# Optimization experiments

Measured on AMD Instinct MI355X. Metric: run time of the kernel, lower is better.

Reference implementation:

```python
import jax, jax.numpy as jnp
import numpy as np

EMBED_DIM = 1024
NUM_HEADS = 16
HEAD_DIM = EMBED_DIM // NUM_HEADS
ROPE_BASE = 10000.0


def rotate_half(x):
    # interleaved variant: pairs (x0,x1) -> (-x1, x0)
    x1 = x[..., ::2]
    x2 = x[..., 1::2]
    return jnp.stack((-x2, x1), axis=-1).reshape(x.shape)


def rope_tables(T, dim, dtype):
    inv_freq = 1.0 / (ROPE_BASE ** (jnp.arange(0, dim, 2, dtype=jnp.float32) / dim))
    t = jnp.arange(T, dtype=jnp.float32)
    freqs = t[:, None] * inv_freq[None, :]          # [T, dim/2]
    emb = jnp.concatenate((freqs, freqs), axis=-1)  # [T, dim]
    return jnp.cos(emb).astype(dtype), jnp.sin(emb).astype(dtype)


def setup_inputs() -> dict:
    key = jax.random.key(0)
    kx, kq, ko = jax.random.split(key, 3)
    B, T, D = 2, 2048, EMBED_DIM
    x = jax.random.normal(kx, (B, T, D), dtype=jnp.float32)
    s = 1.0 / np.sqrt(D)
    Wqkv = jax.random.normal(kq, (D, 3 * D), dtype=jnp.float32) * s
    Wout = jax.random.normal(ko, (D, D), dtype=jnp.float32) * s
    return {"x": x, "Wqkv": Wqkv, "Wout": Wout}


def reference(x, Wqkv, Wout):
    B, T, D = x.shape
    H, hd = NUM_HEADS, HEAD_DIM
    qkv = x @ Wqkv                                   # [B,T,3D]
    q, k, v = jnp.split(qkv, 3, axis=-1)
    q = q.reshape(B, T, H, hd).transpose(0, 2, 1, 3)  # [B,H,T,hd]
    k = k.reshape(B, T, H, hd).transpose(0, 2, 1, 3)
    v = v.reshape(B, T, H, hd).transpose(0, 2, 1, 3)
    cos, sin = rope_tables(T, hd, x.dtype)           # [T,hd]
    cos = cos[None, None, :, :]
    sin = sin[None, None, :, :]
    q = q * cos + rotate_half(q) * sin
    k = k * cos + rotate_half(k) * sin
    scale = 1.0 / np.sqrt(hd).astype(np.float32)
    attn = jnp.einsum('bhtd,bhsd->bhts', q, k) * scale  # [B,H,T,T]
    attn = jax.nn.softmax(attn, axis=-1)
    out = jnp.einsum('bhts,bhsd->bhtd', attn, v)     # [B,H,T,hd]
    out = out.transpose(0, 2, 1, 3).reshape(B, T, D)
    return out @ Wout
```

## Files before the change

### kernel.cpp

```cpp
#include <hip/hip_runtime.h>
#include <hip/hip_bf16.h>
#include <stdint.h>


typedef unsigned short u16;
typedef short bf16x8 __attribute__((ext_vector_type(8)));
typedef float f32x4  __attribute__((ext_vector_type(4)));

#if defined(__has_builtin) && __has_builtin(__builtin_amdgcn_exp2f)
#define EXP2F(x) __builtin_amdgcn_exp2f(x)
#else
#define EXP2F(x) exp2f(x)
#endif

__device__ __forceinline__ u16 f2b(float f) {
  uint32_t u = __float_as_uint(f);
  u += 0x7fffu + ((u >> 16) & 1u);
  return (u16)(u >> 16);
}
__device__ __forceinline__ uint32_t pk2(float a, float b) {
  return (uint32_t)f2b(a) | ((uint32_t)f2b(b) << 16);
}
__device__ __forceinline__ uint32_t pkbf(float a, float b) {
  __hip_bfloat162 h = __float22bfloat162_rn(make_float2(a, b));
  union { __hip_bfloat162 h2; uint32_t u; } cv; cv.h2 = h;
  return cv.u;
}

__device__ __forceinline__ void gl2lds16(const void* g, void* l) {
  __builtin_amdgcn_global_load_lds(
      (const __attribute__((address_space(1))) unsigned int*)g,
      (__attribute__((address_space(3))) unsigned int*)l, 16, 0, 0);
}

__global__ void sniff_kernel(const u16* x, int* flag) {
  __shared__ int cnt;
  if (threadIdx.x == 0) cnt = 0;
  __syncthreads();
  int c = 0;
  for (int i = threadIdx.x; i < 4096; i += 256) {
    float a = fabsf(__uint_as_float(((uint32_t)x[2*i]) << 16));
    if (a > 1e-3f && a < 100.f) c++;
  }
  atomicAdd(&cnt, c);
  __syncthreads();
  if (threadIdx.x == 0) *flag = (cnt > 2048) ? 1 : 0;
}

__device__ __forceinline__ void tr_tile(const void* src, u16* dst, int Kd, int N,
                                        int n0, int k0, int isb, u16* Lt, int tid)
{
  const int r = tid >> 2, cseg = (tid & 3) << 4;
  u16 t[16];
  if (isb) {
    const u16* s = (const u16*)src + (size_t)(k0 + r) * N + n0 + cseg;
    *(uint4*)&t[0] = *(const uint4*)s;
    *(uint4*)&t[8] = *(const uint4*)(s + 8);
  } else {
    const float* s = (const float*)src + (size_t)(k0 + r) * N + n0 + cseg;
    #pragma unroll
    for (int j = 0; j < 4; j++) {
      float4 v = *(const float4*)(s + j * 4);
      t[j*4+0] = f2b(v.x); t[j*4+1] = f2b(v.y); t[j*4+2] = f2b(v.z); t[j*4+3] = f2b(v.w);
    }
  }
  #pragma unroll
  for (int j = 0; j < 16; j++) Lt[(cseg + j) * 72 + r] = t[j];
  __syncthreads();
  const int n = tid >> 2, kseg = (tid & 3) << 4;
  uint4 u0 = *(const uint4*)&Lt[n * 72 + kseg];
  uint4 u1 = *(const uint4*)&Lt[n * 72 + kseg + 8];
  u16* d = dst + (size_t)(n0 + n) * Kd + k0 + kseg;
  *(uint4*)d = u0;
  *(uint4*)(d + 8) = u1;
}

__global__ __launch_bounds__(256) void prep_kernel(
    const void* __restrict__ x, const void* __restrict__ wqkv,
    const void* __restrict__ wout, const int* __restrict__ flag,
    u16* __restrict__ Xb, u16* __restrict__ Wqkvt, u16* __restrict__ Woutt,
    float2* __restrict__ CS)
{
  __shared__ u16 Lt[64 * 72];
  const int isb = *flag;
  const int bid = blockIdx.x, tid = threadIdx.x;
  if (bid < 2048) {
    const size_t i = ((size_t)bid * 256 + tid) * 8;
    if (isb) {
      *(uint4*)&Xb[i] = *(const uint4*)((const u16*)x + i);
    } else {
      const float* s = (const float*)x + i;
      float4 a = *(const float4*)s, b = *(const float4*)(s + 4);
      uint4 p;
      p.x = pkbf(a.x, a.y); p.y = pkbf(a.z, a.w);
      p.z = pkbf(b.x, b.y); p.w = pkbf(b.z, b.w);
      *(uint4*)&Xb[i] = p;
    }
  } else if (bid < 2816) {
    const int b = bid - 2048;
    tr_tile(wqkv, Wqkvt, 1024, 3072, (b % 48) * 64, (b / 48) * 64, isb, Lt, tid);
  } else if (bid < 3072) {
    const int b = bid - 2816;
    tr_tile(wout, Woutt, 1024, 1024, (b % 16) * 64, (b / 16) * 64, isb, Lt, tid);
  } else {
    const int idx = (bid - 3072) * 256 + tid;
    const int t = idx >> 5, f = idx & 31;
    float invf = __expf(-(float)f * 0.2878231366242557f);
    float th = (float)t * invf;
    float sn, cs;
    sincosf(th, &sn, &cs);
    CS[idx] = make_float2(cs, sn);
  }
}

__global__ __launch_bounds__(256) void qkv_kernel(
    const u16* __restrict__ Xb, const u16* __restrict__ Wt,
    const float2* __restrict__ CS,
    u16* __restrict__ Q, u16* __restrict__ K, u16* __restrict__ Vt)
{
  __shared__ u16 As[128 * 64];
  __shared__ u16 Bs[128 * 64];
  const int tid = threadIdx.x;
  const int n0 = blockIdx.x * 128;
  const int m0 = blockIdx.y * 128;
  const int w = tid >> 6, l = tid & 63, lr = l & 15, lq = l >> 4;
  const int mrow0 = (w & 1) * 64;
  const int ncol0 = (w >> 1) * 64;
  const int srow = tid >> 3;
  const int gseg = (tid & 7) ^ (srow & 7);

  f32x4 acc[4][4] = {};

  for (int k0 = 0; k0 < 1024; k0 += 64) {
    __syncthreads();
    #pragma unroll
    for (int rd = 0; rd < 4; rd++) {
      const int row = srow + rd * 32;
      gl2lds16(Xb + (size_t)(m0 + row) * 1024 + k0 + gseg * 8, &As[tid * 8 + rd * 2048]);
      gl2lds16(Wt + (size_t)(n0 + row) * 1024 + k0 + gseg * 8, &Bs[tid * 8 + rd * 2048]);
    }
    __syncthreads();
    #pragma unroll
    for (int kc = 0; kc < 2; kc++) {
      bf16x8 af[4], bf[4];
      #pragma unroll
      for (int i = 0; i < 4; i++) {
        const int seg = ((kc << 2) | lq) ^ (lr & 7);
        af[i] = *(const bf16x8*)&As[(mrow0 + i * 16 + lr) * 64 + seg * 8];
        bf[i] = *(const bf16x8*)&Bs[(ncol0 + i * 16 + lr) * 64 + seg * 8];
      }
      #pragma unroll
      for (int mb = 0; mb < 4; mb++)
        #pragma unroll
        for (int nb = 0; nb < 4; nb++)
          acc[mb][nb] = __builtin_amdgcn_mfma_f32_16x16x32_bf16(af[mb], bf[nb], acc[mb][nb], 0, 0, 0);
    }
  }

  const int col0 = n0 + ncol0;
  const int sec = col0 >> 10;
  const int h = (col0 >> 6) & 15;
  if (sec == 2) {
    #pragma unroll
    for (int mb = 0; mb < 4; mb++) {
      const int row0 = m0 + mrow0 + mb * 16 + lq * 4;
      const int b = row0 >> 11, t0 = row0 & 2047;
      #pragma unroll
      for (int nb = 0; nb < 4; nb++) {
        const int d = nb * 16 + lr;
        uint2 uv;
        uv.x = pkbf(acc[mb][nb][0], acc[mb][nb][1]);
        uv.y = pkbf(acc[mb][nb][2], acc[mb][nb][3]);
        *(uint2*)&Vt[(((size_t)b * 16 + h) * 64 + d) * 2048 + t0] = uv;
      }
    }
  } else {
    u16* dst = (sec == 0) ? Q : K;
    const float qscale = 0.125f * 1.44269504f;
    #pragma unroll
    for (int mb = 0; mb < 4; mb++) {
      const int row0 = m0 + mrow0 + mb * 16 + lq * 4;
      const int b = row0 >> 11, t0 = row0 & 2047;
      #pragma unroll
      for (int nb = 0; nb < 4; nb++) {
        const int d = nb * 16 + lr;
        const int f = d & 31;
        #pragma unroll
        for (int r = 0; r < 4; r++) {
          const int t = t0 + r;
          float2 cs = CS[t * 32 + f];
          float val = acc[mb][nb][r];
          float prt = __shfl_xor(val, 1, 64);
          float res = fmaf(val, cs.x, ((d & 1) ? prt : -prt) * cs.y);
          if (sec == 0) res *= qscale;
          dst[(((size_t)b * 16 + h) * 2048 + t) * 64 + d] = f2b(res);
        }
      }
    }
  }
}

__global__ __launch_bounds__(256, 2) void attn_kernel(
    const u16* __restrict__ Q, const u16* __restrict__ K,
    const u16* __restrict__ Vt, u16* __restrict__ ATT,
    float* __restrict__ Op, float* __restrict__ Ls)
{
  __shared__ u16 Ks[2][64 * 64];
  __shared__ u16 Vs[2][64 * 64];
  __shared__ u16 Ps[4][64 * 64];
  const int tid = threadIdx.x;
  const int w = tid >> 6, l = tid & 63, lr = l & 15, lq = l >> 4;
  const int bh = blockIdx.x >> 3;
  const int qt = blockIdx.x & 7;
  const int ns = gridDim.y, sh = blockIdx.y;
  const int slen = 2048 / ns;
  const int sbeg = sh * slen;
  const size_t base = (size_t)bh * (2048 * 64);
  const int qrow0 = qt * 256 + w * 64;
  u16* Psw = &Ps[w][0];

  bf16x8 qf[4][2];
  #pragma unroll
  for (int mb = 0; mb < 4; mb++)
    #pragma unroll
    for (int kc = 0; kc < 2; kc++)
      qf[mb][kc] = *(const bf16x8*)(Q + base + (size_t)(qrow0 + mb * 16 + lr) * 64 + kc * 32 + lq * 8);

  f32x4 oa[4][4] = {};
  float lsum[4] = {0.f, 0.f, 0.f, 0.f};

  const int srow = tid >> 3;

  auto stage = [&](int buf, int s0) {
    #pragma unroll
    for (int rd = 0; rd < 2; rd++) {
      const int row = srow + rd * 32;
      const int gs = (tid & 7) ^ (row & 7);
      gl2lds16(K + base + (size_t)(s0 + row) * 64 + gs * 8, &Ks[buf][tid * 8 + rd * 2048]);
      gl2lds16(Vt + base + (size_t)row * 2048 + s0 + gs * 8, &Vs[buf][tid * 8 + rd * 2048]);
    }
  };

  stage(0, sbeg);
  const int nt = slen >> 6;

  #pragma unroll 1
  for (int t = 0; t < nt; t++) {
    const int buf = t & 1;
    __syncthreads();
    if (t + 1 < nt) stage(buf ^ 1, sbeg + (t + 1) * 64);

    bf16x8 kf[4][2], vf[4][2];
    #pragma unroll
    for (int nb = 0; nb < 4; nb++)
      #pragma unroll
      for (int kc = 0; kc < 2; kc++) {
        const int seg = ((kc << 2) | lq) ^ (lr & 7);
        kf[nb][kc] = *(const bf16x8*)&Ks[buf][(nb * 16 + lr) * 64 + seg * 8];
        vf[nb][kc] = *(const bf16x8*)&Vs[buf][(nb * 16 + lr) * 64 + seg * 8];
      }

    #pragma unroll
    for (int sb = 0; sb < 4; sb++) {
      #pragma unroll
      for (int mb = 0; mb < 4; mb++) {
        f32x4 st = {};
        st = __builtin_amdgcn_mfma_f32_16x16x32_bf16(kf[sb][0], qf[mb][0], st, 0, 0, 0);
        st = __builtin_amdgcn_mfma_f32_16x16x32_bf16(kf[sb][1], qf[mb][1], st, 0, 0, 0);
        float e0 = EXP2F(st[0]), e1 = EXP2F(st[1]), e2 = EXP2F(st[2]), e3 = EXP2F(st[3]);
        lsum[mb] += (e0 + e1) + (e2 + e3);
        uint2 pp;
        pp.x = pkbf(e0, e1);
        pp.y = pkbf(e2, e3);
        const int pseg = ((sb << 1) | (lq >> 1)) ^ (lr & 7);
        *(uint2*)&Psw[(mb * 16 + lr) * 64 + pseg * 8 + (lq & 1) * 4] = pp;
      }
    }

    #pragma unroll
    for (int mb = 0; mb < 4; mb++) {
      const int rs0 = lq ^ (lr & 7);
      const int rs1 = (4 | lq) ^ (lr & 7);
      bf16x8 pf0 = *(const bf16x8*)&Psw[(mb * 16 + lr) * 64 + rs0 * 8];
      bf16x8 pf1 = *(const bf16x8*)&Psw[(mb * 16 + lr) * 64 + rs1 * 8];
      #pragma unroll
      for (int db = 0; db < 4; db++) {
        oa[db][mb] = __builtin_amdgcn_mfma_f32_16x16x32_bf16(vf[db][0], pf0, oa[db][mb], 0, 0, 0);
        oa[db][mb] = __builtin_amdgcn_mfma_f32_16x16x32_bf16(vf[db][1], pf1, oa[db][mb], 0, 0, 0);
      }
    }
  }

  #pragma unroll
  for (int mb = 0; mb < 4; mb++) {
    float v = lsum[mb];
    v += __shfl_xor(v, 16, 64);
    v += __shfl_xor(v, 32, 64);
    lsum[mb] = v;
  }

  const int b = bh >> 4, h = bh & 15;
  if (ns == 1) {
    #pragma unroll
    for (int mb = 0; mb < 4; mb++) {
      const float inv = 1.f / lsum[mb];
      const int t = qrow0 + mb * 16 + lr;
      u16* dst = ATT + ((size_t)(b * 2048 + t)) * 1024 + h * 64;
      #pragma unroll
      for (int db = 0; db < 4; db++) {
        uint2 u;
        u.x = pkbf(oa[db][mb][0] * inv, oa[db][mb][1] * inv);
        u.y = pkbf(oa[db][mb][2] * inv, oa[db][mb][3] * inv);
        *(uint2*)&dst[db * 16 + lq * 4] = u;
      }
    }
  } else {
    float* op = Op + (size_t)sh * (65536ull * 64);
    #pragma unroll
    for (int mb = 0; mb < 4; mb++) {
      const size_t row = (size_t)bh * 2048 + qrow0 + mb * 16 + lr;
      #pragma unroll
      for (int db = 0; db < 4; db++)
        *(f32x4*)&op[row * 64 + db * 16 + lq * 4] = oa[db][mb];
      if (lq == 0) Ls[(size_t)sh * 65536 + row] = lsum[mb];
    }
  }
}

__global__ __launch_bounds__(256) void combine_kernel(
    const float* __restrict__ Op, const float* __restrict__ Ls, u16* __restrict__ ATT)
{
  const int idx = blockIdx.x * 256 + threadIdx.x;
  const int R = idx >> 3;
  const int c = (idx & 7) * 8;
  const float* p0 = Op + (size_t)R * 64 + c;
  const float* p1 = p0 + 65536ull * 64;
  f32x4 a0 = *(const f32x4*)p0, a1 = *(const f32x4*)(p0 + 4);
  f32x4 b0 = *(const f32x4*)p1, b1 = *(const f32x4*)(p1 + 4);
  const float inv = 1.f / (Ls[R] + Ls[65536 + R]);
  const int bh = R >> 11, trow = R & 2047;
  const int b = bh >> 4, h = bh & 15;
  u16* d = ATT + ((size_t)(b * 2048 + trow)) * 1024 + h * 64 + c;
  uint4 u;
  u.x = pkbf((a0[0] + b0[0]) * inv, (a0[1] + b0[1]) * inv);
  u.y = pkbf((a0[2] + b0[2]) * inv, (a0[3] + b0[3]) * inv);
  u.z = pkbf((a1[0] + b1[0]) * inv, (a1[1] + b1[1]) * inv);
  u.w = pkbf((a1[2] + b1[2]) * inv, (a1[3] + b1[3]) * inv);
  *(uint4*)d = u;
}

__global__ __launch_bounds__(256) void outproj_kernel(
    const u16* __restrict__ A, const u16* __restrict__ Wt,
    const int* __restrict__ flag, void* __restrict__ outv)
{
  __shared__ u16 As[128 * 64];
  __shared__ u16 Bs[128 * 64];
  const int isb = *flag;
  const int tid = threadIdx.x;
  const int n0 = blockIdx.x * 128;
  const int m0 = blockIdx.y * 128;
  const int w = tid >> 6, l = tid & 63, lr = l & 15, lq = l >> 4;
  const int mrow0 = (w & 1) * 64;
  const int ncol0 = (w >> 1) * 64;
  const int srow = tid >> 3;
  const int gseg = (tid & 7) ^ (srow & 7);

  f32x4 acc[4][4] = {};

  for (int k0 = 0; k0 < 1024; k0 += 64) {
    __syncthreads();
    #pragma unroll
    for (int rd = 0; rd < 4; rd++) {
      const int row = srow + rd * 32;
      gl2lds16(A + (size_t)(m0 + row) * 1024 + k0 + gseg * 8, &As[tid * 8 + rd * 2048]);
      gl2lds16(Wt + (size_t)(n0 + row) * 1024 + k0 + gseg * 8, &Bs[tid * 8 + rd * 2048]);
    }
    __syncthreads();
    #pragma unroll
    for (int kc = 0; kc < 2; kc++) {
      bf16x8 af[4], bf[4];
      #pragma unroll
      for (int i = 0; i < 4; i++) {
        const int seg = ((kc << 2) | lq) ^ (lr & 7);
        af[i] = *(const bf16x8*)&As[(mrow0 + i * 16 + lr) * 64 + seg * 8];
        bf[i] = *(const bf16x8*)&Bs[(ncol0 + i * 16 + lr) * 64 + seg * 8];
      }
      #pragma unroll
      for (int mb = 0; mb < 4; mb++)
        #pragma unroll
        for (int nb = 0; nb < 4; nb++)
          acc[mb][nb] = __builtin_amdgcn_mfma_f32_16x16x32_bf16(af[mb], bf[nb], acc[mb][nb], 0, 0, 0);
    }
  }
  #pragma unroll
  for (int mb = 0; mb < 4; mb++) {
    const int row = m0 + mrow0 + mb * 16 + lq * 4;
    #pragma unroll
    for (int nb = 0; nb < 4; nb++) {
      const int col = n0 + ncol0 + nb * 16 + lr;
      #pragma unroll
      for (int r = 0; r < 4; r++) {
        float val = acc[mb][nb][r];
        if (isb) ((u16*)outv)[(size_t)(row + r) * 1024 + col] = f2b(val);
        else     ((float*)outv)[(size_t)(row + r) * 1024 + col] = val;
      }
    }
  }
}

extern "C" void kernel_launch(void* const* d_in, const int* in_sizes, int n_in,
                              void* d_out, int out_size, void* d_ws, size_t ws_size,
                              hipStream_t stream)
{
  const void* x    = d_in[0];
  const void* wqkv = d_in[1];
  const void* wout = d_in[2];
  char* ws = (char*)d_ws;
  const size_t MB = 1024 * 1024;
  int*    flag   = (int*)ws;
  float2* CS     = (float2*)(ws + 1024);
  u16*    Xb     = (u16*)(ws + 1 * MB);
  u16*    ATT    = Xb;
  u16*    Wqkvt  = (u16*)(ws + 9 * MB);
  u16*    Woutt  = (u16*)(ws + 15 * MB);
  u16*    Q      = (u16*)(ws + 17 * MB);
  u16*    K      = (u16*)(ws + 25 * MB);
  u16*    Vt     = (u16*)(ws + 33 * MB);
  float*  Op     = (float*)(ws + 41 * MB);
  float*  Ls     = (float*)(ws + 75 * MB);

  const bool split = ws_size >= 76 * MB;
  const int ns = split ? 2 : 1;

  sniff_kernel<<<1, 256, 0, stream>>>((const u16*)x, flag);
  prep_kernel<<<3328, 256, 0, stream>>>(x, wqkv, wout, flag, Xb, Wqkvt, Woutt, CS);
  qkv_kernel<<<dim3(24, 32), 256, 0, stream>>>(Xb, Wqkvt, CS, Q, K, Vt);
  attn_kernel<<<dim3(256, ns), 256, 0, stream>>>(Q, K, Vt, ATT, Op, Ls);
  if (split)
    combine_kernel<<<2048, 256, 0, stream>>>(Op, Ls, ATT);
  outproj_kernel<<<dim3(8, 32), 256, 0, stream>>>(ATT, Woutt, flag, d_out);
}
```

Measured before the change: 214.6 us.

## Fuse split-KV combine into out-projection, shrink attention tiles, skip bf16 copy

Removes the separate combine kernel by having a new out-projection kernel read both partial attention outputs and row sums, normalize them, and write bf16 tiles straight into LDS as the GEMM A operand. The attention kernel now uses 32 query rows per wave (128 per block), launches twice as many blocks, halves the P scratch in LDS and asks for 3 blocks per CU. Block indexing is reordered so that consecutive blocks cover different heads. When the input is already bf16, the QKV GEMM reads x directly and skips the copy in prep. The costs are that the out-projection rereads fp32 partials once per N-tile (8 times), and that smaller attention tiles give less MFMA reuse of each K/V tile.

```diff
diff --git a/kernel.cpp b/kernel.cpp
--- a/kernel.cpp
+++ b/kernel.cpp
@@ -17,9 +17,6 @@
   uint32_t u = __float_as_uint(f);
   u += 0x7fffu + ((u >> 16) & 1u);
   return (u16)(u >> 16);
-}
-__device__ __forceinline__ uint32_t pk2(float a, float b) {
-  return (uint32_t)f2b(a) | ((uint32_t)f2b(b) << 16);
 }
 __device__ __forceinline__ uint32_t pkbf(float a, float b) {
   __hip_bfloat162 h = __float22bfloat162_rn(make_float2(a, b));
@@ -85,17 +82,14 @@
   const int isb = *flag;
   const int bid = blockIdx.x, tid = threadIdx.x;
   if (bid < 2048) {
+    if (isb) return;
     const size_t i = ((size_t)bid * 256 + tid) * 8;
-    if (isb) {
-      *(uint4*)&Xb[i] = *(const uint4*)((const u16*)x + i);
-    } else {
-      const float* s = (const float*)x + i;
-      float4 a = *(const float4*)s, b = *(const float4*)(s + 4);
-      uint4 p;
-      p.x = pkbf(a.x, a.y); p.y = pkbf(a.z, a.w);
-      p.z = pkbf(b.x, b.y); p.w = pkbf(b.z, b.w);
-      *(uint4*)&Xb[i] = p;
-    }
+    const float* s = (const float*)x + i;
+    float4 a = *(const float4*)s, b = *(const float4*)(s + 4);
+    uint4 p;
+    p.x = pkbf(a.x, a.y); p.y = pkbf(a.z, a.w);
+    p.z = pkbf(b.x, b.y); p.w = pkbf(b.z, b.w);
+    *(uint4*)&Xb[i] = p;
   } else if (bid < 2816) {
     const int b = bid - 2048;
     tr_tile(wqkv, Wqkvt, 1024, 3072, (b % 48) * 64, (b / 48) * 64, isb, Lt, tid);
@@ -114,12 +108,14 @@
 }
 
 __global__ __launch_bounds__(256) void qkv_kernel(
-    const u16* __restrict__ Xb, const u16* __restrict__ Wt,
+    const void* __restrict__ xraw, const u16* __restrict__ Xb,
+    const u16* __restrict__ Wt, const int* __restrict__ flag,
     const float2* __restrict__ CS,
     u16* __restrict__ Q, u16* __restrict__ K, u16* __restrict__ Vt)
 {
   __shared__ u16 As[128 * 64];
   __shared__ u16 Bs[128 * 64];
+  const u16* Asrc = (*flag) ? (const u16*)xraw : Xb;
   const int tid = threadIdx.x;
   const int n0 = blockIdx.x * 128;
   const int m0 = blockIdx.y * 128;
@@ -136,7 +132,7 @@
     #pragma unroll
     for (int rd = 0; rd < 4; rd++) {
       const int row = srow + rd * 32;
-      gl2lds16(Xb + (size_t)(m0 + row) * 1024 + k0 + gseg * 8, &As[tid * 8 + rd * 2048]);
+      gl2lds16(Asrc + (size_t)(m0 + row) * 1024 + k0 + gseg * 8, &As[tid * 8 + rd * 2048]);
       gl2lds16(Wt + (size_t)(n0 + row) * 1024 + k0 + gseg * 8, &Bs[tid * 8 + rd * 2048]);
     }
     __syncthreads();
@@ -200,34 +196,34 @@
   }
 }
 
-__global__ __launch_bounds__(256, 2) void attn_kernel(
+__global__ __launch_bounds__(256, 3) void attn_kernel(
     const u16* __restrict__ Q, const u16* __restrict__ K,
     const u16* __restrict__ Vt, u16* __restrict__ ATT,
     float* __restrict__ Op, float* __restrict__ Ls)
 {
   __shared__ u16 Ks[2][64 * 64];
   __shared__ u16 Vs[2][64 * 64];
-  __shared__ u16 Ps[4][64 * 64];
+  __shared__ u16 Ps[4][32 * 64];
   const int tid = threadIdx.x;
   const int w = tid >> 6, l = tid & 63, lr = l & 15, lq = l >> 4;
-  const int bh = blockIdx.x >> 3;
-  const int qt = blockIdx.x & 7;
+  const int bh = blockIdx.x & 31;
+  const int qt = blockIdx.x >> 5;
   const int ns = gridDim.y, sh = blockIdx.y;
   const int slen = 2048 / ns;
   const int sbeg = sh * slen;
   const size_t base = (size_t)bh * (2048 * 64);
-  const int qrow0 = qt * 256 + w * 64;
+  const int qrow0 = qt * 128 + w * 32;
   u16* Psw = &Ps[w][0];
 
-  bf16x8 qf[4][2];
+  bf16x8 qf[2][2];
   #pragma unroll
-  for (int mb = 0; mb < 4; mb++)
+  for (int mb = 0; mb < 2; mb++)
     #pragma unroll
     for (int kc = 0; kc < 2; kc++)
       qf[mb][kc] = *(const bf16x8*)(Q + base + (size_t)(qrow0 + mb * 16 + lr) * 64 + kc * 32 + lq * 8);
 
-  f32x4 oa[4][4] = {};
-  float lsum[4] = {0.f, 0.f, 0.f, 0.f};
+  f32x4 oa[4][2] = {};
+  float2 ls2[2] = {};
 
   const int srow = tid >> 3;
 
@@ -263,12 +259,13 @@
     #pragma unroll
     for (int sb = 0; sb < 4; sb++) {
       #pragma unroll
-      for (int mb = 0; mb < 4; mb++) {
+      for (int mb = 0; mb < 2; mb++) {
         f32x4 st = {};
         st = __builtin_amdgcn_mfma_f32_16x16x32_bf16(kf[sb][0], qf[mb][0], st, 0, 0, 0);
         st = __builtin_amdgcn_mfma_f32_16x16x32_bf16(kf[sb][1], qf[mb][1], st, 0, 0, 0);
         float e0 = EXP2F(st[0]), e1 = EXP2F(st[1]), e2 = EXP2F(st[2]), e3 = EXP2F(st[3]);
-        lsum[mb] += (e0 + e1) + (e2 + e3);
+        ls2[mb].x += e0 + e2;
+        ls2[mb].y += e1 + e3;
         uint2 pp;
         pp.x = pkbf(e0, e1);
         pp.y = pkbf(e2, e3);
@@ -278,7 +275,7 @@
     }
 
     #pragma unroll
-    for (int mb = 0; mb < 4; mb++) {
+    for (int mb = 0; mb < 2; mb++) {
       const int rs0 = lq ^ (lr & 7);
       const int rs1 = (4 | lq) ^ (lr & 7);
       bf16x8 pf0 = *(const bf16x8*)&Psw[(mb * 16 + lr) * 64 + rs0 * 8];
@@ -291,9 +288,10 @@
     }
   }
 
+  float lsum[2];
   #pragma unroll
-  for (int mb = 0; mb < 4; mb++) {
-    float v = lsum[mb];
+  for (int mb = 0; mb < 2; mb++) {
+    float v = ls2[mb].x + ls2[mb].y;
     v += __shfl_xor(v, 16, 64);
     v += __shfl_xor(v, 32, 64);
     lsum[mb] = v;
@@ -302,7 +300,7 @@
   const int b = bh >> 4, h = bh & 15;
   if (ns == 1) {
     #pragma unroll
-    for (int mb = 0; mb < 4; mb++) {
+    for (int mb = 0; mb < 2; mb++) {
       const float inv = 1.f / lsum[mb];
       const int t = qrow0 + mb * 16 + lr;
       u16* dst = ATT + ((size_t)(b * 2048 + t)) * 1024 + h * 64;
@@ -317,7 +315,7 @@
   } else {
     float* op = Op + (size_t)sh * (65536ull * 64);
     #pragma unroll
-    for (int mb = 0; mb < 4; mb++) {
+    for (int mb = 0; mb < 2; mb++) {
       const size_t row = (size_t)bh * 2048 + qrow0 + mb * 16 + lr;
       #pragma unroll
       for (int db = 0; db < 4; db++)
@@ -327,26 +325,87 @@
   }
 }
 
-__global__ __launch_bounds__(256) void combine_kernel(
-    const float* __restrict__ Op, const float* __restrict__ Ls, u16* __restrict__ ATT)
-{
-  const int idx = blockIdx.x * 256 + threadIdx.x;
-  const int R = idx >> 3;
-  const int c = (idx & 7) * 8;
-  const float* p0 = Op + (size_t)R * 64 + c;
-  const float* p1 = p0 + 65536ull * 64;
-  f32x4 a0 = *(const f32x4*)p0, a1 = *(const f32x4*)(p0 + 4);
-  f32x4 b0 = *(const f32x4*)p1, b1 = *(const f32x4*)(p1 + 4);
-  const float inv = 1.f / (Ls[R] + Ls[65536 + R]);
-  const int bh = R >> 11, trow = R & 2047;
-  const int b = bh >> 4, h = bh & 15;
-  u16* d = ATT + ((size_t)(b * 2048 + trow)) * 1024 + h * 64 + c;
-  uint4 u;
-  u.x = pkbf((a0[0] + b0[0]) * inv, (a0[1] + b0[1]) * inv);
-  u.y = pkbf((a0[2] + b0[2]) * inv, (a0[3] + b0[3]) * inv);
-  u.z = pkbf((a1[0] + b1[0]) * inv, (a1[1] + b1[1]) * inv);
-  u.w = pkbf((a1[2] + b1[2]) * inv, (a1[3] + b1[3]) * inv);
-  *(uint4*)d = u;
+__global__ __launch_bounds__(256) void outproj2_kernel(
+    const float* __restrict__ Op, const float* __restrict__ Ls,
+    const u16* __restrict__ Wt, const int* __restrict__ flag,
+    void* __restrict__ outv)
+{
+  __shared__ u16 As[128 * 64];
+  __shared__ u16 Bs[128 * 64];
+  const int isb = *flag;
+  const int tid = threadIdx.x;
+  const int n0 = blockIdx.x * 128;
+  const int m0 = blockIdx.y * 128;
+  const int w = tid >> 6, l = tid & 63, lr = l & 15, lq = l >> 4;
+  const int mrow0 = (w & 1) * 64;
+  const int ncol0 = (w >> 1) * 64;
+  const int srow = tid >> 3;
+  const int gseg = (tid & 7) ^ (srow & 7);
+  const int rloc = tid >> 1, hf = tid & 1;
+  const int grow = m0 + rloc;
+  const int gb = grow >> 11, gt = grow & 2047;
+
+  f32x4 acc[4][4] = {};
+
+  for (int k0 = 0; k0 < 1024; k0 += 64) {
+    const int h = k0 >> 6;
+    __syncthreads();
+    #pragma unroll
+    for (int rd = 0; rd < 4; rd++) {
+      const int row = srow + rd * 32;
+      gl2lds16(Wt + (size_t)(n0 + row) * 1024 + k0 + gseg * 8, &Bs[tid * 8 + rd * 2048]);
+    }
+    {
+      const size_t RR = ((size_t)(gb * 16 + h)) * 2048 + gt;
+      const float inv = 1.f / (Ls[RR] + Ls[65536 + RR]);
+      const float* p0 = Op + RR * 64 + hf * 32;
+      const float* p1 = p0 + 65536ull * 64;
+      #pragma unroll
+      for (int j = 0; j < 4; j++) {
+        f32x4 a0 = *(const f32x4*)(p0 + j * 8);
+        f32x4 a1 = *(const f32x4*)(p0 + j * 8 + 4);
+        f32x4 b0 = *(const f32x4*)(p1 + j * 8);
+        f32x4 b1 = *(const f32x4*)(p1 + j * 8 + 4);
+        uint4 u;
+        u.x = pkbf((a0[0] + b0[0]) * inv, (a0[1] + b0[1]) * inv);
+        u.y = pkbf((a0[2] + b0[2]) * inv, (a0[3] + b0[3]) * inv);
+        u.z = pkbf((a1[0] + b1[0]) * inv, (a1[1] + b1[1]) * inv);
+        u.w = pkbf((a1[2] + b1[2]) * inv, (a1[3] + b1[3]) * inv);
+        const int g = hf * 4 + j;
+        *(uint4*)&As[rloc * 64 + (g ^ (rloc & 7)) * 8] = u;
+      }
+    }
+    __syncthreads();
+    #pragma unroll
+    for (int kc = 0; kc < 2; kc++) {
+      bf16x8 af[4], bf[4];
+      #pragma unroll
+      for (int i = 0; i < 4; i++) {
+        const int seg = ((kc << 2) | lq) ^ (lr & 7);
+        af[i] = *(const bf16x8*)&As[(mrow0 + i * 16 + lr) * 64 + seg * 8];
+        bf[i] = *(const bf16x8*)&Bs[(ncol0 + i * 16 + lr) * 64 + seg * 8];
+      }
+      #pragma unroll
+      for (int mb = 0; mb < 4; mb++)
+        #pragma unroll
+        for (int nb = 0; nb < 4; nb++)
+          acc[mb][nb] = __builtin_amdgcn_mfma_f32_16x16x32_bf16(af[mb], bf[nb], acc[mb][nb], 0, 0, 0);
+    }
+  }
+  #pragma unroll
+  for (int mb = 0; mb < 4; mb++) {
+    const int row = m0 + mrow0 + mb * 16 + lq * 4;
+    #pragma unroll
+    for (int nb = 0; nb < 4; nb++) {
+      const int col = n0 + ncol0 + nb * 16 + lr;
+      #pragma unroll
+      for (int r = 0; r < 4; r++) {
+        float val = acc[mb][nb][r];
+        if (isb) ((u16*)outv)[(size_t)(row + r) * 1024 + col] = f2b(val);
+        else     ((float*)outv)[(size_t)(row + r) * 1024 + col] = val;
+      }
+    }
+  }
 }
 
 __global__ __launch_bounds__(256) void outproj_kernel(
@@ -434,9 +493,10 @@
 
   sniff_kernel<<<1, 256, 0, stream>>>((const u16*)x, flag);
   prep_kernel<<<3328, 256, 0, stream>>>(x, wqkv, wout, flag, Xb, Wqkvt, Woutt, CS);
-  qkv_kernel<<<dim3(24, 32), 256, 0, stream>>>(Xb, Wqkvt, CS, Q, K, Vt);
-  attn_kernel<<<dim3(256, ns), 256, 0, stream>>>(Q, K, Vt, ATT, Op, Ls);
+  qkv_kernel<<<dim3(24, 32), 256, 0, stream>>>(x, Xb, Wqkvt, flag, CS, Q, K, Vt);
+  attn_kernel<<<dim3(512, ns), 256, 0, stream>>>(Q, K, Vt, ATT, Op, Ls);
   if (split)
-    combine_kernel<<<2048, 256, 0, stream>>>(Op, Ls, ATT);
-  outproj_kernel<<<dim3(8, 32), 256, 0, stream>>>(ATT, Woutt, flag, d_out);
-}
+    outproj2_kernel<<<dim3(8, 32), 256, 0, stream>>>(Op, Ls, Woutt, flag, d_out);
+  else
+    outproj_kernel<<<dim3(8, 32), 256, 0, stream>>>(ATT, Woutt, flag, d_out);
+}
```

Result: slower. 244.2 us (+13.8%).

## Fuse all stages into one persistent cooperative kernel with grid syncs

Applied to the files above, without the earlier changes.

Merges the sniff, prep, QKV GEMM, attention, combine and out-projection launches into a single cooperative persistent kernel whose blocks loop over virtual tiles, separated by grid-wide syncs. This removes launch gaps and the flag round-trip, and skips the X copy when the input is already bf16. Attention tiles shrink to 128 query rows (32 per wave) so three blocks fit per CU with shared LDS. Grid barriers and reduced per-wave work may cut efficiency in the GEMM and attention phases.

```diff
diff --git a/kernel.cpp b/kernel.cpp
--- a/kernel.cpp
+++ b/kernel.cpp
@@ -1,7 +1,10 @@
 #include <hip/hip_runtime.h>
 #include <hip/hip_bf16.h>
+#include <hip/hip_cooperative_groups.h>
 #include <stdint.h>
 
+
+namespace cg = cooperative_groups;
 
 typedef unsigned short u16;
 typedef short bf16x8 __attribute__((ext_vector_type(8)));
@@ -18,9 +21,6 @@
   u += 0x7fffu + ((u >> 16) & 1u);
   return (u16)(u >> 16);
 }
-__device__ __forceinline__ uint32_t pk2(float a, float b) {
-  return (uint32_t)f2b(a) | ((uint32_t)f2b(b) << 16);
-}
 __device__ __forceinline__ uint32_t pkbf(float a, float b) {
   __hip_bfloat162 h = __float22bfloat162_rn(make_float2(a, b));
   union { __hip_bfloat162 h2; uint32_t u; } cv; cv.h2 = h;
@@ -31,20 +31,6 @@
   __builtin_amdgcn_global_load_lds(
       (const __attribute__((address_space(1))) unsigned int*)g,
       (__attribute__((address_space(3))) unsigned int*)l, 16, 0, 0);
-}
-
-__global__ void sniff_kernel(const u16* x, int* flag) {
-  __shared__ int cnt;
-  if (threadIdx.x == 0) cnt = 0;
-  __syncthreads();
-  int c = 0;
-  for (int i = threadIdx.x; i < 4096; i += 256) {
-    float a = fabsf(__uint_as_float(((uint32_t)x[2*i]) << 16));
-    if (a > 1e-3f && a < 100.f) c++;
-  }
-  atomicAdd(&cnt, c);
-  __syncthreads();
-  if (threadIdx.x == 0) *flag = (cnt > 2048) ? 1 : 0;
 }
 
 __device__ __forceinline__ void tr_tile(const void* src, u16* dst, int Kd, int N,
@@ -75,54 +61,14 @@
   *(uint4*)(d + 8) = u1;
 }
 
-__global__ __launch_bounds__(256) void prep_kernel(
-    const void* __restrict__ x, const void* __restrict__ wqkv,
-    const void* __restrict__ wout, const int* __restrict__ flag,
-    u16* __restrict__ Xb, u16* __restrict__ Wqkvt, u16* __restrict__ Woutt,
-    float2* __restrict__ CS)
-{
-  __shared__ u16 Lt[64 * 72];
-  const int isb = *flag;
-  const int bid = blockIdx.x, tid = threadIdx.x;
-  if (bid < 2048) {
-    const size_t i = ((size_t)bid * 256 + tid) * 8;
-    if (isb) {
-      *(uint4*)&Xb[i] = *(const uint4*)((const u16*)x + i);
-    } else {
-      const float* s = (const float*)x + i;
-      float4 a = *(const float4*)s, b = *(const float4*)(s + 4);
-      uint4 p;
-      p.x = pkbf(a.x, a.y); p.y = pkbf(a.z, a.w);
-      p.z = pkbf(b.x, b.y); p.w = pkbf(b.z, b.w);
-      *(uint4*)&Xb[i] = p;
-    }
-  } else if (bid < 2816) {
-    const int b = bid - 2048;
-    tr_tile(wqkv, Wqkvt, 1024, 3072, (b % 48) * 64, (b / 48) * 64, isb, Lt, tid);
-  } else if (bid < 3072) {
-    const int b = bid - 2816;
-    tr_tile(wout, Woutt, 1024, 1024, (b % 16) * 64, (b / 16) * 64, isb, Lt, tid);
-  } else {
-    const int idx = (bid - 3072) * 256 + tid;
-    const int t = idx >> 5, f = idx & 31;
-    float invf = __expf(-(float)f * 0.2878231366242557f);
-    float th = (float)t * invf;
-    float sn, cs;
-    sincosf(th, &sn, &cs);
-    CS[idx] = make_float2(cs, sn);
-  }
-}
-
-__global__ __launch_bounds__(256) void qkv_kernel(
-    const u16* __restrict__ Xb, const u16* __restrict__ Wt,
+__device__ __forceinline__ void qkv_tile(
+    const u16* __restrict__ Asrc, const u16* __restrict__ Wt,
     const float2* __restrict__ CS,
-    u16* __restrict__ Q, u16* __restrict__ K, u16* __restrict__ Vt)
-{
-  __shared__ u16 As[128 * 64];
-  __shared__ u16 Bs[128 * 64];
-  const int tid = threadIdx.x;
-  const int n0 = blockIdx.x * 128;
-  const int m0 = blockIdx.y * 128;
+    u16* __restrict__ Q, u16* __restrict__ K, u16* __restrict__ Vt,
+    u16* smem, int n0, int m0, int tid)
+{
+  u16* As = smem;
+  u16* Bs = smem + 8192;
   const int w = tid >> 6, l = tid & 63, lr = l & 15, lq = l >> 4;
   const int mrow0 = (w & 1) * 64;
   const int ncol0 = (w >> 1) * 64;
@@ -136,7 +82,7 @@
     #pragma unroll
     for (int rd = 0; rd < 4; rd++) {
       const int row = srow + rd * 32;
-      gl2lds16(Xb + (size_t)(m0 + row) * 1024 + k0 + gseg * 8, &As[tid * 8 + rd * 2048]);
+      gl2lds16(Asrc + (size_t)(m0 + row) * 1024 + k0 + gseg * 8, &As[tid * 8 + rd * 2048]);
       gl2lds16(Wt + (size_t)(n0 + row) * 1024 + k0 + gseg * 8, &Bs[tid * 8 + rd * 2048]);
     }
     __syncthreads();
@@ -200,34 +146,33 @@
   }
 }
 
-__global__ __launch_bounds__(256, 2) void attn_kernel(
+__device__ __forceinline__ void attn_tile(
     const u16* __restrict__ Q, const u16* __restrict__ K,
     const u16* __restrict__ Vt, u16* __restrict__ ATT,
-    float* __restrict__ Op, float* __restrict__ Ls)
-{
-  __shared__ u16 Ks[2][64 * 64];
-  __shared__ u16 Vs[2][64 * 64];
-  __shared__ u16 Ps[4][64 * 64];
-  const int tid = threadIdx.x;
+    float* __restrict__ Op, float* __restrict__ Ls,
+    u16* smem, int bh, int qt, int sh, int ns, int tid)
+{
+  u16* Ks = smem;
+  u16* Vs = smem + 8192;
+  u16* Ps = smem + 16384;
   const int w = tid >> 6, l = tid & 63, lr = l & 15, lq = l >> 4;
-  const int bh = blockIdx.x >> 3;
-  const int qt = blockIdx.x & 7;
-  const int ns = gridDim.y, sh = blockIdx.y;
   const int slen = 2048 / ns;
   const int sbeg = sh * slen;
   const size_t base = (size_t)bh * (2048 * 64);
-  const int qrow0 = qt * 256 + w * 64;
-  u16* Psw = &Ps[w][0];
-
-  bf16x8 qf[4][2];
+  const int qrow0 = qt * 128 + w * 32;
+  u16* Psw = Ps + w * (32 * 64);
+
+  __syncthreads();
+
+  bf16x8 qf[2][2];
   #pragma unroll
-  for (int mb = 0; mb < 4; mb++)
+  for (int mb = 0; mb < 2; mb++)
     #pragma unroll
     for (int kc = 0; kc < 2; kc++)
       qf[mb][kc] = *(const bf16x8*)(Q + base + (size_t)(qrow0 + mb * 16 + lr) * 64 + kc * 32 + lq * 8);
 
-  f32x4 oa[4][4] = {};
-  float lsum[4] = {0.f, 0.f, 0.f, 0.f};
+  f32x4 oa[4][2] = {};
+  float2 ls2[2] = {};
 
   const int srow = tid >> 3;
 
@@ -236,8 +181,8 @@
     for (int rd = 0; rd < 2; rd++) {
       const int row = srow + rd * 32;
       const int gs = (tid & 7) ^ (row & 7);
-      gl2lds16(K + base + (size_t)(s0 + row) * 64 + gs * 8, &Ks[buf][tid * 8 + rd * 2048]);
-      gl2lds16(Vt + base + (size_t)row * 2048 + s0 + gs * 8, &Vs[buf][tid * 8 + rd * 2048]);
+      gl2lds16(K + base + (size_t)(s0 + row) * 64 + gs * 8, &Ks[buf * 4096 + tid * 8 + rd * 2048]);
+      gl2lds16(Vt + base + (size_t)row * 2048 + s0 + gs * 8, &Vs[buf * 4096 + tid * 8 + rd * 2048]);
     }
   };
 
@@ -256,19 +201,20 @@
       #pragma unroll
       for (int kc = 0; kc < 2; kc++) {
         const int seg = ((kc << 2) | lq) ^ (lr & 7);
-        kf[nb][kc] = *(const bf16x8*)&Ks[buf][(nb * 16 + lr) * 64 + seg * 8];
-        vf[nb][kc] = *(const bf16x8*)&Vs[buf][(nb * 16 + lr) * 64 + seg * 8];
+        kf[nb][kc] = *(const bf16x8*)&Ks[buf * 4096 + (nb * 16 + lr) * 64 + seg * 8];
+        vf[nb][kc] = *(const bf16x8*)&Vs[buf * 4096 + (nb * 16 + lr) * 64 + seg * 8];
       }
 
     #pragma unroll
     for (int sb = 0; sb < 4; sb++) {
       #pragma unroll
-      for (int mb = 0; mb < 4; mb++) {
+      for (int mb = 0; mb < 2; mb++) {
         f32x4 st = {};
         st = __builtin_amdgcn_mfma_f32_16x16x32_bf16(kf[sb][0], qf[mb][0], st, 0, 0, 0);
         st = __builtin_amdgcn_mfma_f32_16x16x32_bf16(kf[sb][1], qf[mb][1], st, 0, 0, 0);
         float e0 = EXP2F(st[0]), e1 = EXP2F(st[1]), e2 = EXP2F(st[2]), e3 = EXP2F(st[3]);
-        lsum[mb] += (e0 + e1) + (e2 + e3);
+        ls2[mb].x += e0 + e2;
+        ls2[mb].y += e1 + e3;
         uint2 pp;
         pp.x = pkbf(e0, e1);
         pp.y = pkbf(e2, e3);
@@ -278,7 +224,7 @@
     }
 
     #pragma unroll
-    for (int mb = 0; mb < 4; mb++) {
+    for (int mb = 0; mb < 2; mb++) {
       const int rs0 = lq ^ (lr & 7);
       const int rs1 = (4 | lq) ^ (lr & 7);
       bf16x8 pf0 = *(const bf16x8*)&Psw[(mb * 16 + lr) * 64 + rs0 * 8];
@@ -291,9 +237,10 @@
     }
   }
 
+  float lsum[2];
   #pragma unroll
-  for (int mb = 0; mb < 4; mb++) {
-    float v = lsum[mb];
+  for (int mb = 0; mb < 2; mb++) {
+    float v = ls2[mb].x + ls2[mb].y;
     v += __shfl_xor(v, 16, 64);
     v += __shfl_xor(v, 32, 64);
     lsum[mb] = v;
@@ -302,7 +249,7 @@
   const int b = bh >> 4, h = bh & 15;
   if (ns == 1) {
     #pragma unroll
-    for (int mb = 0; mb < 4; mb++) {
+    for (int mb = 0; mb < 2; mb++) {
       const float inv = 1.f / lsum[mb];
       const int t = qrow0 + mb * 16 + lr;
       u16* dst = ATT + ((size_t)(b * 2048 + t)) * 1024 + h * 64;
@@ -317,7 +264,7 @@
   } else {
     float* op = Op + (size_t)sh * (65536ull * 64);
     #pragma unroll
-    for (int mb = 0; mb < 4; mb++) {
+    for (int mb = 0; mb < 2; mb++) {
       const size_t row = (size_t)bh * 2048 + qrow0 + mb * 16 + lr;
       #pragma unroll
       for (int db = 0; db < 4; db++)
@@ -327,38 +274,12 @@
   }
 }
 
-__global__ __launch_bounds__(256) void combine_kernel(
-    const float* __restrict__ Op, const float* __restrict__ Ls, u16* __restrict__ ATT)
-{
-  const int idx = blockIdx.x * 256 + threadIdx.x;
-  const int R = idx >> 3;
-  const int c = (idx & 7) * 8;
-  const float* p0 = Op + (size_t)R * 64 + c;
-  const float* p1 = p0 + 65536ull * 64;
-  f32x4 a0 = *(const f32x4*)p0, a1 = *(const f32x4*)(p0 + 4);
-  f32x4 b0 = *(const f32x4*)p1, b1 = *(const f32x4*)(p1 + 4);
-  const float inv = 1.f / (Ls[R] + Ls[65536 + R]);
-  const int bh = R >> 11, trow = R & 2047;
-  const int b = bh >> 4, h = bh & 15;
-  u16* d = ATT + ((size_t)(b * 2048 + trow)) * 1024 + h * 64 + c;
-  uint4 u;
-  u.x = pkbf((a0[0] + b0[0]) * inv, (a0[1] + b0[1]) * inv);
-  u.y = pkbf((a0[2] + b0[2]) * inv, (a0[3] + b0[3]) * inv);
-  u.z = pkbf((a1[0] + b1[0]) * inv, (a1[1] + b1[1]) * inv);
-  u.w = pkbf((a1[2] + b1[2]) * inv, (a1[3] + b1[3]) * inv);
-  *(uint4*)d = u;
-}
-
-__global__ __launch_bounds__(256) void outproj_kernel(
+__device__ __forceinline__ void outproj_tile(
     const u16* __restrict__ A, const u16* __restrict__ Wt,
-    const int* __restrict__ flag, void* __restrict__ outv)
-{
-  __shared__ u16 As[128 * 64];
-  __shared__ u16 Bs[128 * 64];
-  const int isb = *flag;
-  const int tid = threadIdx.x;
-  const int n0 = blockIdx.x * 128;
-  const int m0 = blockIdx.y * 128;
+    int isb, void* __restrict__ outv, u16* smem, int n0, int m0, int tid)
+{
+  u16* As = smem;
+  u16* Bs = smem + 8192;
   const int w = tid >> 6, l = tid & 63, lr = l & 15, lq = l >> 4;
   const int mrow0 = (w & 1) * 64;
   const int ncol0 = (w >> 1) * 64;
@@ -408,6 +329,104 @@
   }
 }
 
+__global__ __launch_bounds__(256, 3) void mega_kernel(
+    const void* __restrict__ x, const void* __restrict__ wqkv,
+    const void* __restrict__ wout,
+    u16* __restrict__ Xb, u16* __restrict__ Wqkvt, u16* __restrict__ Woutt,
+    float2* __restrict__ CS, u16* __restrict__ Q, u16* __restrict__ K,
+    u16* __restrict__ Vt, u16* __restrict__ ATT,
+    float* __restrict__ Op, float* __restrict__ Ls,
+    void* __restrict__ outv, int ns)
+{
+  __shared__ __align__(16) u16 smem[24576];
+  cg::grid_group gg = cg::this_grid();
+  const int tid = threadIdx.x;
+  const int bid = blockIdx.x;
+  const int gsz = gridDim.x;
+
+  int isb;
+  {
+    int* cnt = (int*)smem;
+    if (tid == 0) *cnt = 0;
+    __syncthreads();
+    int c = 0;
+    for (int i = tid; i < 4096; i += 256) {
+      float a = fabsf(__uint_as_float(((uint32_t)((const u16*)x)[2 * i]) << 16));
+      if (a > 1e-3f && a < 100.f) c++;
+    }
+    atomicAdd(cnt, c);
+    __syncthreads();
+    isb = (*cnt > 2048) ? 1 : 0;
+  }
+
+  for (int vb = bid; vb < 3328; vb += gsz) {
+    __syncthreads();
+    if (vb < 2048) {
+      if (isb) continue;
+      const size_t i = ((size_t)vb * 256 + tid) * 8;
+      const float* s = (const float*)x + i;
+      float4 a = *(const float4*)s, b = *(const float4*)(s + 4);
+      uint4 p;
+      p.x = pkbf(a.x, a.y); p.y = pkbf(a.z, a.w);
+      p.z = pkbf(b.x, b.y); p.w = pkbf(b.z, b.w);
+      *(uint4*)&Xb[i] = p;
+    } else if (vb < 2816) {
+      const int b = vb - 2048;
+      tr_tile(wqkv, Wqkvt, 1024, 3072, (b % 48) * 64, (b / 48) * 64, isb, smem, tid);
+    } else if (vb < 3072) {
+      const int b = vb - 2816;
+      tr_tile(wout, Woutt, 1024, 1024, (b % 16) * 64, (b / 16) * 64, isb, smem, tid);
+    } else {
+      const int idx = (vb - 3072) * 256 + tid;
+      const int t = idx >> 5, f = idx & 31;
+      float invf = __expf(-(float)f * 0.2878231366242557f);
+      float th = (float)t * invf;
+      float sn, cs;
+      sincosf(th, &sn, &cs);
+      CS[idx] = make_float2(cs, sn);
+    }
+  }
+  gg.sync();
+
+  {
+    const u16* Asrc = isb ? (const u16*)x : Xb;
+    for (int vb = bid; vb < 768; vb += gsz)
+      qkv_tile(Asrc, Wqkvt, CS, Q, K, Vt, smem, (vb % 24) * 128, (vb / 24) * 128, tid);
+  }
+  gg.sync();
+
+  for (int vb = bid; vb < 512 * ns; vb += gsz) {
+    const int r = vb & 511;
+    attn_tile(Q, K, Vt, ATT, Op, Ls, smem, r & 31, r >> 5, vb >> 9, ns, tid);
+  }
+  gg.sync();
+
+  if (ns == 2) {
+    for (int idx = bid * 256 + tid; idx < 524288; idx += gsz * 256) {
+      const int R = idx >> 3;
+      const int c = (idx & 7) * 8;
+      const float* p0 = Op + (size_t)R * 64 + c;
+      const float* p1 = p0 + 65536ull * 64;
+      f32x4 a0 = *(const f32x4*)p0, a1 = *(const f32x4*)(p0 + 4);
+      f32x4 b0 = *(const f32x4*)p1, b1 = *(const f32x4*)(p1 + 4);
+      const float inv = 1.f / (Ls[R] + Ls[65536 + R]);
+      const int bh = R >> 11, trow = R & 2047;
+      const int b = bh >> 4, h = bh & 15;
+      u16* d = ATT + ((size_t)(b * 2048 + trow)) * 1024 + h * 64 + c;
+      uint4 u;
+      u.x = pkbf((a0[0] + b0[0]) * inv, (a0[1] + b0[1]) * inv);
+      u.y = pkbf((a0[2] + b0[2]) * inv, (a0[3] + b0[3]) * inv);
+      u.z = pkbf((a1[0] + b1[0]) * inv, (a1[1] + b1[1]) * inv);
+      u.w = pkbf((a1[2] + b1[2]) * inv, (a1[3] + b1[3]) * inv);
+      *(uint4*)d = u;
+    }
+  }
+  gg.sync();
+
+  for (int vb = bid; vb < 256; vb += gsz)
+    outproj_tile(ATT, Woutt, isb, outv, smem, (vb & 7) * 128, (vb >> 3) * 128, tid);
+}
+
 extern "C" void kernel_launch(void* const* d_in, const int* in_sizes, int n_in,
                               void* d_out, int out_size, void* d_ws, size_t ws_size,
                               hipStream_t stream)
@@ -417,7 +436,6 @@
   const void* wout = d_in[2];
   char* ws = (char*)d_ws;
   const size_t MB = 1024 * 1024;
-  int*    flag   = (int*)ws;
   float2* CS     = (float2*)(ws + 1024);
   u16*    Xb     = (u16*)(ws + 1 * MB);
   u16*    ATT    = Xb;
@@ -429,14 +447,21 @@
   float*  Op     = (float*)(ws + 41 * MB);
   float*  Ls     = (float*)(ws + 75 * MB);
 
-  const bool split = ws_size >= 76 * MB;
-  const int ns = split ? 2 : 1;
-
-  sniff_kernel<<<1, 256, 0, stream>>>((const u16*)x, flag);
-  prep_kernel<<<3328, 256, 0, stream>>>(x, wqkv, wout, flag, Xb, Wqkvt, Woutt, CS);
-  qkv_kernel<<<dim3(24, 32), 256, 0, stream>>>(Xb, Wqkvt, CS, Q, K, Vt);
-  attn_kernel<<<dim3(256, ns), 256, 0, stream>>>(Q, K, Vt, ATT, Op, Ls);
-  if (split)
-    combine_kernel<<<2048, 256, 0, stream>>>(Op, Ls, ATT);
-  outproj_kernel<<<dim3(8, 32), 256, 0, stream>>>(ATT, Woutt, flag, d_out);
-}
+  int ns = (ws_size >= 76 * MB) ? 2 : 1;
+
+  int nb = 0;
+  hipOccupancyMaxActiveBlocksPerMultiprocessor(&nb, mega_kernel, 256, 0);
+  if (nb < 1) nb = 1;
+  int grid = nb * 256;
+  if (grid > 768) grid = 768;
+
+  void* outv = d_out;
+  void* kargs[] = {
+    (void*)&x, (void*)&wqkv, (void*)&wout,
+    (void*)&Xb, (void*)&Wqkvt, (void*)&Woutt, (void*)&CS,
+    (void*)&Q, (void*)&K, (void*)&Vt, (void*)&ATT,
+    (void*)&Op, (void*)&Ls, (void*)&outv, (void*)&ns
+  };
+  hipLaunchCooperativeKernel((const void*)mega_kernel, dim3(grid), dim3(256),
+                             kargs, 0, stream);
+}
```

Measured after the change: 380.5 us. 77.3% more time.
